# Optimization experiments

Hardware: AMD Instinct MI355X
Metric: run time of the kernel (lower is better)

The kernel has to match this reference:

```python
import jax, jax.numpy as jnp
import numpy as np

B, S, U, H, NT, MEM, FF = 2, 1024, 1024, 16, 32000, 576, 4096
D = U // H
VOCAB = 1024  # AdaptiveEmbedding(input_dim=units) in source -> vocab == units


def setup_inputs() -> dict:
    key = jax.random.key(0)
    ks = jax.random.split(key, 12)
    w = lambda k, shp, s=0.02: jax.random.normal(k, shp, jnp.float32) * s
    return dict(
        tokens=jax.random.randint(ks[0], (B, S), 0, VOCAB, dtype=jnp.int32),
        memory=jax.random.normal(ks[1], (B, MEM, U), jnp.float32),  # HelixMemory state (n_turns+memory_len)
        embed_table=w(ks[2], (VOCAB, U)),
        Wq=w(ks[3], (U, U)), Wkv=w(ks[4], (U, 2 * U)), Wr=w(ks[5], (U, U)), Wo=w(ks[6], (U, U)),
        bq=jnp.zeros((U,), jnp.float32), bkv=jnp.zeros((2 * U,), jnp.float32),
        br=jnp.zeros((U,), jnp.float32), bo=jnp.zeros((U,), jnp.float32),
        bias_context=w(ks[7], (U,)), bias_relative=w(ks[8], (U,)),
        ln1_g=jnp.ones((U,), jnp.float32), ln1_b=jnp.zeros((U,), jnp.float32),
        W1=w(ks[9], (U, FF)), b1=jnp.zeros((FF,), jnp.float32),
        W2=w(ks[10], (FF, U)), b2=jnp.zeros((U,), jnp.float32),
        ln2_g=jnp.ones((U,), jnp.float32), ln2_b=jnp.zeros((U,), jnp.float32),
        Wout=w(ks[11], (U, NT)), bout=jnp.zeros((NT,), jnp.float32),
    )


def _layer_norm(x, g, b, eps=1e-5):
    mu = jnp.mean(x, -1, keepdims=True)
    var = jnp.var(x, -1, keepdims=True)
    return (x - mu) * jax.lax.rsqrt(var + eps) * g + b


def _pos_embed(k_len, d):
    # Transformer-XL sinusoidal relative positions, descending k_len-1 .. 0
    pos = jnp.arange(k_len - 1, -1, -1, dtype=jnp.float32)
    inv_freq = 1.0 / (10000.0 ** (jnp.arange(0, d, 2, dtype=jnp.float32) / d))
    sinusoid = pos[:, None] * inv_freq[None, :]  # (k_len, d/2)
    return jnp.concatenate([jnp.sin(sinusoid), jnp.cos(sinusoid)], -1)  # (k_len, d)


def _rel_shift(x):
    # standard Transformer-XL relative shift: (B,H,S,K) -> shifted (B,H,S,K)
    b, h, s, k = x.shape
    x = jnp.pad(x, ((0, 0), (0, 0), (0, 0), (1, 0)))
    x = x.reshape(b, h, k + 1, s)[:, :, 1:, :]
    return x.reshape(b, h, s, k)


def _forward(tokens, memory, embed_table, Wq, Wkv, Wr, Wo, bq, bkv, br, bo,
             bias_context, bias_relative, ln1_g, ln1_b, W1, b1, W2, b2,
             ln2_g, ln2_b, Wout, bout):
    x = embed_table[tokens] * jnp.sqrt(jnp.float32(U))     # (B,S,U) embed + Scale
    full = jnp.concatenate([memory, x], axis=1)            # (B,K,U) memory-augmented keys/values
    k_len = full.shape[1]
    rel = _pos_embed(k_len, U)                             # (K,U) positional embedding

    q = x @ Wq + bq                                        # (B,S,U)
    kv = full @ Wkv + bkv                                  # (B,K,2U)
    r = (rel @ Wr + br).reshape(k_len, H, D)               # (K,H,D)
    k = kv[..., :U].reshape(B, k_len, H, D)
    v = kv[..., U:].reshape(B, k_len, H, D)
    q_c = (q + bias_context).reshape(B, S, H, D)           # q + u
    q_r = (q + bias_relative).reshape(B, S, H, D)          # q + v

    a_c = jnp.einsum('bihd,bjhd->bhij', q_c, k)            # content scores
    a_r = _rel_shift(jnp.einsum('bihd,jhd->bhij', q_r, r)) # position scores, rel-shifted
    att = (a_c + a_r) / jnp.sqrt(jnp.float32(D))
    # causal mask with memory offset: query i may attend keys j <= i + MEM
    mask = jnp.arange(k_len)[None, :] <= (jnp.arange(S)[:, None] + (k_len - S))
    att = jnp.where(mask[None, None], att, jnp.float32(-1e30))
    att = jax.nn.softmax(att, axis=-1)
    out = jnp.einsum('bhij,bjhd->bihd', att, v).reshape(B, S, U)
    out = out @ Wo + bo

    h1 = _layer_norm(x + out, ln1_g, ln1_b)                # Add + LayerNorm
    ff = jax.nn.relu(h1 @ W1 + b1) @ W2 + b2               # FeedForward
    h2 = _layer_norm(h1 + ff, ln2_g, ln2_b)
    return jax.nn.softmax(h2 @ Wout + bout, axis=-1)       # AdaptiveSoftmax head (div_val=1)


def reference(tokens, memory, embed_table, Wq, Wkv, Wr, Wo, bq, bkv, br, bo,
              bias_context, bias_relative, ln1_g, ln1_b, W1, b1, W2, b2,
              ln2_g, ln2_b, Wout, bout):
    return _forward(tokens, memory, embed_table, Wq, Wkv, Wr, Wo, bq, bkv, br, bo,
                    bias_context, bias_relative, ln1_g, ln1_b, W1, b1, W2, b2,
                    ln2_g, ln2_b, Wout, bout)
```

## Files before the change

kernel.cpp:

```cpp
#include <hip/hip_runtime.h>
#include <stdint.h>

typedef unsigned short u16;
typedef __bf16 bf16x8 __attribute__((ext_vector_type(8)));
typedef float f32x4 __attribute__((ext_vector_type(4)));

#define AS1 __attribute__((address_space(1)))
#define AS3 __attribute__((address_space(3)))

enum {
  B_ = 2, S_ = 1024, U_ = 1024, H_ = 16, D_ = 64,
  NT_ = 32000, MEM_ = 576, FF_ = 4096, KL_ = 1600,
  BS_ = 2048, BKL_ = 3200
};

__device__ __forceinline__ u16 f2b(float f) {
  uint32_t u = __builtin_bit_cast(uint32_t, f);
  u = (u + 0x7fffu + ((u >> 16) & 1u)) >> 16;
  return (u16)u;
}
__device__ __forceinline__ float b2f(u16 h) {
  uint32_t u = ((uint32_t)h) << 16;
  return __builtin_bit_cast(float, u);
}

__device__ __forceinline__ float block_sum(float v, volatile float* red) {
  int lane = threadIdx.x & 63, wv = threadIdx.x >> 6;
#pragma unroll
  for (int o = 32; o; o >>= 1) v += __shfl_xor(v, o, 64);
  if (lane == 0) red[wv] = v;
  __syncthreads();
  v = red[0] + red[1] + red[2] + red[3];
  __syncthreads();
  return v;
}
__device__ __forceinline__ float block_max(float v, volatile float* red) {
  int lane = threadIdx.x & 63, wv = threadIdx.x >> 6;
#pragma unroll
  for (int o = 32; o; o >>= 1) v = fmaxf(v, __shfl_xor(v, o, 64));
  if (lane == 0) red[wv] = v;
  __syncthreads();
  v = fmaxf(fmaxf(red[0], red[1]), fmaxf(red[2], red[3]));
  __syncthreads();
  return v;
}

__global__ __launch_bounds__(256)
void k_gemm(const u16* __restrict__ A, const u16* __restrict__ Bt,
            float* __restrict__ Cf, u16* __restrict__ Cb,
            const float* __restrict__ bias,
            int M, int N, int K, int lda, int ldb, int ldc,
            long long sAb, long long sAh, long long sBb, long long sBh,
            long long sCb, long long sCh, int nh, int mode)
{
  __shared__ __align__(16) u16 As[128][64];
  __shared__ __align__(16) u16 Bs[128][64];

  int z = blockIdx.z;
  int bb = z / nh, hh = z - bb * nh;
  A  += bb * sAb + hh * sAh;
  Bt += bb * sBb + hh * sBh;
  long long coff = bb * sCb + hh * sCh;

  int m0 = blockIdx.y * 128, n0 = blockIdx.x * 128;
  int t = threadIdx.x;
  int lane = t & 63, wave = t >> 6;
  int wm = (wave >> 1) * 64, wn = (wave & 1) * 64;
  int lrow = lane & 15, lq = lane >> 4;

  int srow = t >> 3;
  int scol = (t & 7) * 8;

  f32x4 acc[4][4];
#pragma unroll
  for (int i = 0; i < 4; i++)
#pragma unroll
    for (int j = 0; j < 4; j++) acc[i][j] = (f32x4){0.f, 0.f, 0.f, 0.f};

  for (int k0 = 0; k0 < K; k0 += 64) {
#pragma unroll
    for (int it = 0; it < 4; ++it) {
      int r = srow + 32 * it;
      int gr = m0 + r;
      if (gr < M)
        __builtin_amdgcn_global_load_lds(
            (const AS1 void*)(A + (long long)gr * lda + k0 + scol),
            (AS3 void*)(&As[r][scol]), 16, 0, 0);
      int gn = n0 + r;
      if (gn < N)
        __builtin_amdgcn_global_load_lds(
            (const AS1 void*)(Bt + (long long)gn * ldb + k0 + scol),
            (AS3 void*)(&Bs[r][scol]), 16, 0, 0);
    }
    __syncthreads();
#pragma unroll
    for (int ks = 0; ks < 2; ++ks) {
      int kk = ks * 32 + lq * 8;
      bf16x8 av[4], bv[4];
#pragma unroll
      for (int i = 0; i < 4; i++) av[i] = *(const bf16x8*)(&As[wm + i * 16 + lrow][kk]);
#pragma unroll
      for (int j = 0; j < 4; j++) bv[j] = *(const bf16x8*)(&Bs[wn + j * 16 + lrow][kk]);
#pragma unroll
      for (int i = 0; i < 4; i++)
#pragma unroll
        for (int j = 0; j < 4; j++)
          acc[i][j] = __builtin_amdgcn_mfma_f32_16x16x32_bf16(av[i], bv[j], acc[i][j], 0, 0, 0);
    }
    __syncthreads();
  }

#pragma unroll
  for (int j = 0; j < 4; j++) {
    int col = n0 + wn + j * 16 + lrow;
    if (col >= N) continue;
    float bvv = bias ? bias[col] : 0.f;
#pragma unroll
    for (int i = 0; i < 4; i++) {
      int row0 = m0 + wm + i * 16 + lq * 4;
#pragma unroll
      for (int r = 0; r < 4; r++) {
        int gr = row0 + r;
        if (gr >= M) continue;
        float v = acc[i][j][r] + bvv;
        if (mode == 2) {
          int tc = col - (S_ - 1 - gr);
          if (tc >= 0) {
            long long idx = coff + (long long)gr * ldc + tc;
            Cb[idx] = f2b(b2f(Cb[idx]) + v);
          }
          continue;
        }
        if (mode == 1) v = fmaxf(v, 0.f);
        long long idx = coff + (long long)gr * ldc + col;
        if (Cf) Cf[idx] = v;
        if (Cb) Cb[idx] = f2b(v);
      }
    }
  }
}

__global__ void k_embed(const int* __restrict__ tokens, const float* __restrict__ memory,
                        const float* __restrict__ table, u16* __restrict__ fullbf,
                        u16* __restrict__ xbf, float* __restrict__ xf)
{
  int row = blockIdx.x;
  int b = row / KL_, jk = row - b * KL_;
  int c = threadIdx.x * 4;
  u16* dst = fullbf + (size_t)row * U_ + c;
  if (jk < MEM_) {
    float4 v = *(const float4*)(memory + ((size_t)b * MEM_ + jk) * U_ + c);
    dst[0] = f2b(v.x); dst[1] = f2b(v.y); dst[2] = f2b(v.z); dst[3] = f2b(v.w);
  } else {
    int i = jk - MEM_;
    int tok = tokens[b * S_ + i];
    float4 v = *(const float4*)(table + (size_t)tok * U_ + c);
    v.x *= 32.f; v.y *= 32.f; v.z *= 32.f; v.w *= 32.f;
    dst[0] = f2b(v.x); dst[1] = f2b(v.y); dst[2] = f2b(v.z); dst[3] = f2b(v.w);
    size_t xi = ((size_t)b * S_ + i) * U_ + c;
    *(float4*)(xf + xi) = v;
    u16* xd = xbf + xi;
    xd[0] = f2b(v.x); xd[1] = f2b(v.y); xd[2] = f2b(v.z); xd[3] = f2b(v.w);
  }
}

__global__ void k_relpos(u16* __restrict__ relbf)
{
  int m = blockIdx.x;
  float pos = (float)(KL_ - 1 - m);
  const float c0 = 9.210340371976184f / 512.0f;
  for (int c = threadIdx.x; c < U_; c += 256) {
    int i = (c < 512) ? c : (c - 512);
    float inv = expf(-(float)i * c0);
    float arg = pos * inv;
    float v = (c < 512) ? sinf(arg) : cosf(arg);
    relbf[(size_t)m * U_ + c] = f2b(v);
  }
}

__global__ void k_qbias(const float* __restrict__ qf, const float* __restrict__ bc,
                        const float* __restrict__ br, u16* __restrict__ qc,
                        u16* __restrict__ qr)
{
  int c = threadIdx.x * 4;
  size_t idx = (size_t)blockIdx.x * U_ + c;
  float4 q = *(const float4*)(qf + idx);
  float4 vc = *(const float4*)(bc + c);
  float4 vr = *(const float4*)(br + c);
  qc[idx + 0] = f2b(q.x + vc.x); qc[idx + 1] = f2b(q.y + vc.y);
  qc[idx + 2] = f2b(q.z + vc.z); qc[idx + 3] = f2b(q.w + vc.w);
  qr[idx + 0] = f2b(q.x + vr.x); qr[idx + 1] = f2b(q.y + vr.y);
  qr[idx + 2] = f2b(q.z + vr.z); qr[idx + 3] = f2b(q.w + vr.w);
}

__global__ void k_transpose(const float* __restrict__ in, u16* __restrict__ out,
                            int R, int C)
{
  __shared__ float tile[32][33];
  int tx = threadIdx.x & 31, ty = threadIdx.x >> 5;
  int c0 = blockIdx.x * 32, r0 = blockIdx.y * 32;
#pragma unroll
  for (int i = 0; i < 4; i++) {
    int r = r0 + ty + i * 8;
    tile[ty + i * 8][tx] = in[(size_t)r * C + c0 + tx];
  }
  __syncthreads();
#pragma unroll
  for (int i = 0; i < 4; i++) {
    int c = c0 + ty + i * 8;
    out[(size_t)c * R + r0 + tx] = f2b(tile[tx][ty + i * 8]);
  }
}

__global__ void k_vt(const u16* __restrict__ kvbf, u16* __restrict__ vT)
{
  __shared__ u16 tile[32][33];
  int z = blockIdx.z;
  int b = z >> 4, h = z & 15;
  int tx = threadIdx.x & 31, ty = threadIdx.x >> 5;
  int j0 = blockIdx.x * 32, d0 = blockIdx.y * 32;
#pragma unroll
  for (int i = 0; i < 4; i++) {
    int j = j0 + ty + i * 8;
    tile[ty + i * 8][tx] = kvbf[((size_t)(b * KL_ + j)) * (2 * U_) + U_ + h * 64 + d0 + tx];
  }
  __syncthreads();
#pragma unroll
  for (int i = 0; i < 4; i++) {
    int d = d0 + ty + i * 8;
    vT[((size_t)(z * 64 + d)) * KL_ + j0 + tx] = tile[tx][ty + i * 8];
  }
}

__global__ void k_attnsm(u16* __restrict__ C1)
{
  __shared__ float red[4];
  int i = blockIdx.x, z = blockIdx.y;
  size_t base = ((size_t)z * S_ + i) * KL_;
  int jmax = i + MEM_;
  int t = threadIdx.x;
  float vloc[7];
  float lmax = -1e30f;
  int cnt = 0;
  for (int j = t; j < KL_; j += 256, ++cnt) {
    float v = -1e30f;
    if (j <= jmax) v = b2f(C1[base + j]) * 0.125f;
    vloc[cnt] = v;
    lmax = fmaxf(lmax, v);
  }
  float M = block_max(lmax, red);
  float lsum = 0.f;
  for (int c = 0; c < cnt; ++c) lsum += expf(vloc[c] - M);
  float L = block_sum(lsum, red);
  float inv = 1.f / L;
  cnt = 0;
  for (int j = t; j < KL_; j += 256, ++cnt)
    C1[base + j] = f2b(expf(vloc[cnt] - M) * inv);
}

__global__ void k_ln(const float* __restrict__ a, const float* __restrict__ b,
                     const float* __restrict__ g, const float* __restrict__ be,
                     float* __restrict__ yf, u16* __restrict__ yb)
{
  __shared__ float red[4];
  int c = threadIdx.x * 4;
  size_t idx = (size_t)blockIdx.x * U_ + c;
  float4 va = *(const float4*)(a + idx);
  float4 vb = *(const float4*)(b + idx);
  float s0 = va.x + vb.x, s1 = va.y + vb.y, s2 = va.z + vb.z, s3 = va.w + vb.w;
  float sum = block_sum(s0 + s1 + s2 + s3, red);
  float sq  = block_sum(s0 * s0 + s1 * s1 + s2 * s2 + s3 * s3, red);
  float mean = sum * (1.0f / U_);
  float var = sq * (1.0f / U_) - mean * mean;
  float rs = rsqrtf(var + 1e-5f);
  float4 vg = *(const float4*)(g + c);
  float4 vbe = *(const float4*)(be + c);
  float y0 = (s0 - mean) * rs * vg.x + vbe.x;
  float y1 = (s1 - mean) * rs * vg.y + vbe.y;
  float y2 = (s2 - mean) * rs * vg.z + vbe.z;
  float y3 = (s3 - mean) * rs * vg.w + vbe.w;
  if (yf) { float4 o = make_float4(y0, y1, y2, y3); *(float4*)(yf + idx) = o; }
  yb[idx + 0] = f2b(y0); yb[idx + 1] = f2b(y1);
  yb[idx + 2] = f2b(y2); yb[idx + 3] = f2b(y3);
}

__global__ void k_outsm(float* __restrict__ logits)
{
  __shared__ float redm[4], redl[4];
  int row = blockIdx.x, t = threadIdx.x;
  float* lp = logits + (size_t)row * NT_;
  float m = -1e30f, l = 0.f;
  for (int j = t; j < NT_; j += 256) {
    float x = lp[j];
    if (x > m) { l = l * expf(m - x) + 1.f; m = x; }
    else       { l += expf(x - m); }
  }
  int lane = t & 63, wv = t >> 6;
#pragma unroll
  for (int o = 32; o; o >>= 1) {
    float mo = __shfl_xor(m, o, 64), lo = __shfl_xor(l, o, 64);
    float mn = fmaxf(m, mo);
    l = l * expf(m - mn) + lo * expf(mo - mn);
    m = mn;
  }
  if (lane == 0) { redm[wv] = m; redl[wv] = l; }
  __syncthreads();
  float M = fmaxf(fmaxf(redm[0], redm[1]), fmaxf(redm[2], redm[3]));
  float L = redl[0] * expf(redm[0] - M) + redl[1] * expf(redm[1] - M) +
            redl[2] * expf(redm[2] - M) + redl[3] * expf(redm[3] - M);
  float inv = 1.f / L;
  for (int j = t; j < NT_; j += 256)
    lp[j] = expf(lp[j] - M) * inv;
}

static void gemm(hipStream_t st, const u16* A, const u16* Bt, float* Cf, u16* Cb,
                 const float* bias, int M, int N, int K, int lda, int ldb, int ldc,
                 long long sAb, long long sAh, long long sBb, long long sBh,
                 long long sCb, long long sCh, int nb, int nh, int mode)
{
  dim3 g((N + 127) / 128, (M + 127) / 128, nb * nh);
  k_gemm<<<g, 256, 0, st>>>(A, Bt, Cf, Cb, bias, M, N, K, lda, ldb, ldc,
                            sAb, sAh, sBb, sBh, sCb, sCh, nh, mode);
}

extern "C" void kernel_launch(void* const* d_in, const int* in_sizes, int n_in,
                              void* d_out, int out_size, void* d_ws, size_t ws_size,
                              hipStream_t stream)
{
  const int*   tokens = (const int*)d_in[0];
  const float* memory = (const float*)d_in[1];
  const float* table  = (const float*)d_in[2];
  const float* Wq   = (const float*)d_in[3];
  const float* Wkv  = (const float*)d_in[4];
  const float* Wr   = (const float*)d_in[5];
  const float* Wo   = (const float*)d_in[6];
  const float* bq   = (const float*)d_in[7];
  const float* bkv  = (const float*)d_in[8];
  const float* br   = (const float*)d_in[9];
  const float* bo   = (const float*)d_in[10];
  const float* bctx = (const float*)d_in[11];
  const float* brel = (const float*)d_in[12];
  const float* ln1g = (const float*)d_in[13];
  const float* ln1b = (const float*)d_in[14];
  const float* W1   = (const float*)d_in[15];
  const float* b1   = (const float*)d_in[16];
  const float* W2   = (const float*)d_in[17];
  const float* b2   = (const float*)d_in[18];
  const float* ln2g = (const float*)d_in[19];
  const float* ln2b = (const float*)d_in[20];
  const float* Wout = (const float*)d_in[21];
  const float* bout = (const float*)d_in[22];
  float* out = (float*)d_out;

  char* w = (char*)d_ws;
  size_t off = 0;
  auto carve = [&](size_t bytes) -> char* {
    char* p = w + off;
    off = (off + bytes + 255) & ~(size_t)255;
    return p;
  };

  u16*  WqT    = (u16*)carve((size_t)U_ * U_ * 2);
  u16*  WkvT   = (u16*)carve((size_t)2 * U_ * U_ * 2);
  u16*  WrT    = (u16*)carve((size_t)U_ * U_ * 2);
  u16*  WoT    = (u16*)carve((size_t)U_ * U_ * 2);
  u16*  W1T    = (u16*)carve((size_t)FF_ * U_ * 2);
  u16*  W2T    = (u16*)carve((size_t)U_ * FF_ * 2);
  float* xf    = (float*)carve((size_t)BS_ * U_ * 4);
  u16*  xbf    = (u16*)carve((size_t)BS_ * U_ * 2);
  u16*  fullbf = (u16*)carve((size_t)BKL_ * U_ * 2);
  u16*  relbf  = (u16*)carve((size_t)KL_ * U_ * 2);
  float* qf    = (float*)carve((size_t)BS_ * U_ * 4);
  u16*  qcbf   = (u16*)carve((size_t)BS_ * U_ * 2);
  u16*  qrbf   = (u16*)carve((size_t)BS_ * U_ * 2);
  u16*  kvbf   = (u16*)carve((size_t)BKL_ * 2 * U_ * 2);
  u16*  vT     = (u16*)carve((size_t)B_ * H_ * D_ * KL_ * 2);
  u16*  rW     = (u16*)carve((size_t)KL_ * U_ * 2);
  u16*  attout = (u16*)carve((size_t)BS_ * U_ * 2);
  float* of    = (float*)carve((size_t)BS_ * U_ * 4);
  float* h1f   = (float*)carve((size_t)BS_ * U_ * 4);
  u16*  h1bf   = (u16*)carve((size_t)BS_ * U_ * 2);
  u16*  ff1bf  = (u16*)carve((size_t)BS_ * FF_ * 2);
  float* ff2f  = (float*)carve((size_t)BS_ * U_ * 4);
  u16*  h2bf   = (u16*)carve((size_t)BS_ * U_ * 2);

  size_t scoreBytes = (size_t)B_ * H_ * S_ * KL_ * 2;
  char* big = carve(scoreBytes);
  u16* C1    = (u16*)big;
  u16* WoutT = (u16*)big;

  if (off > ws_size) return;

  k_transpose<<<dim3(U_ / 32, U_ / 32), 256, 0, stream>>>(Wq, WqT, U_, U_);
  k_transpose<<<dim3(2 * U_ / 32, U_ / 32), 256, 0, stream>>>(Wkv, WkvT, U_, 2 * U_);
  k_transpose<<<dim3(U_ / 32, U_ / 32), 256, 0, stream>>>(Wr, WrT, U_, U_);
  k_transpose<<<dim3(U_ / 32, U_ / 32), 256, 0, stream>>>(Wo, WoT, U_, U_);
  k_transpose<<<dim3(FF_ / 32, U_ / 32), 256, 0, stream>>>(W1, W1T, U_, FF_);
  k_transpose<<<dim3(U_ / 32, FF_ / 32), 256, 0, stream>>>(W2, W2T, FF_, U_);

  k_embed<<<dim3(BKL_), 256, 0, stream>>>(tokens, memory, table, fullbf, xbf, xf);
  k_relpos<<<dim3(KL_), 256, 0, stream>>>(relbf);

  gemm(stream, xbf, WqT, qf, nullptr, bq, BS_, U_, U_, U_, U_, U_,
       0, 0, 0, 0, 0, 0, 1, 1, 0);
  k_qbias<<<dim3(BS_), 256, 0, stream>>>(qf, bctx, brel, qcbf, qrbf);

  gemm(stream, fullbf, WkvT, nullptr, kvbf, bkv, BKL_, 2 * U_, U_, U_, U_, 2 * U_,
       0, 0, 0, 0, 0, 0, 1, 1, 0);
  k_vt<<<dim3(KL_ / 32, 2, B_ * H_), 256, 0, stream>>>(kvbf, vT);

  gemm(stream, relbf, WrT, nullptr, rW, br, KL_, U_, U_, U_, U_, U_,
       0, 0, 0, 0, 0, 0, 1, 1, 0);

  gemm(stream, qcbf, kvbf, nullptr, C1, nullptr,
       S_, KL_, D_, U_, 2 * U_, KL_,
       (long long)S_ * U_, 64, (long long)KL_ * 2 * U_, 64,
       (long long)H_ * S_ * KL_, (long long)S_ * KL_, B_, H_, 0);
  gemm(stream, qrbf, rW, nullptr, C1, nullptr,
       S_, KL_, D_, U_, U_, KL_,
       (long long)S_ * U_, 64, 0, 64,
       (long long)H_ * S_ * KL_, (long long)S_ * KL_, B_, H_, 2);

  k_attnsm<<<dim3(S_, B_ * H_), 256, 0, stream>>>(C1);

  gemm(stream, C1, vT, nullptr, attout, nullptr,
       S_, D_, KL_, KL_, KL_, U_,
       (long long)H_ * S_ * KL_, (long long)S_ * KL_,
       (long long)H_ * D_ * KL_, (long long)D_ * KL_,
       (long long)S_ * U_, 64, B_, H_, 0);

  gemm(stream, attout, WoT, of, nullptr, bo, BS_, U_, U_, U_, U_, U_,
       0, 0, 0, 0, 0, 0, 1, 1, 0);
  k_ln<<<dim3(BS_), 256, 0, stream>>>(xf, of, ln1g, ln1b, h1f, h1bf);

  gemm(stream, h1bf, W1T, nullptr, ff1bf, b1, BS_, FF_, U_, U_, U_, FF_,
       0, 0, 0, 0, 0, 0, 1, 1, 1);
  gemm(stream, ff1bf, W2T, ff2f, nullptr, b2, BS_, U_, FF_, FF_, FF_, U_,
       0, 0, 0, 0, 0, 0, 1, 1, 0);
  k_ln<<<dim3(BS_), 256, 0, stream>>>(h1f, ff2f, ln2g, ln2b, nullptr, h2bf);

  k_transpose<<<dim3(NT_ / 32, U_ / 32), 256, 0, stream>>>(Wout, WoutT, U_, NT_);

  gemm(stream, h2bf, WoutT, out, nullptr, bout, BS_, NT_, U_, U_, U_, NT_,
       0, 0, 0, 0, 0, 0, 1, 1, 0);
  k_outsm<<<dim3(BS_), 256, 0, stream>>>(out);
}
```

Before: 1.518 ms.

## Skip masked attention tiles and double-buffer LDS in the GEMM kernel

Adds causal tile skipping to the attention path. QK^T tiles lying entirely past the memory-offset causal boundary are skipped, and rel-shift score tiles that would never be written are skipped. The softmax processes only columns up to the block-row's causal limit, and the PV GEMM clamps its K extent to that limit. Separately, the GEMM kernel now double-buffers its LDS tiles so the next k-slice's global-to-LDS loads are issued before the MFMA work on the current slice. This doubles LDS use per block, which may lower occupancy, and relies on unwritten score regions never being read.

```diff
diff --git a/kernel.cpp b/kernel.cpp
--- a/kernel.cpp
+++ b/kernel.cpp
@@ -51,10 +51,16 @@
             const float* __restrict__ bias,
             int M, int N, int K, int lda, int ldb, int ldc,
             long long sAb, long long sAh, long long sBb, long long sBh,
-            long long sCb, long long sCh, int nh, int mode)
-{
-  __shared__ __align__(16) u16 As[128][64];
-  __shared__ __align__(16) u16 Bs[128][64];
+            long long sCb, long long sCh, int nh, int mode,
+            int kclamp_off, int flags)
+{
+  __shared__ __align__(16) u16 As[2][128][64];
+  __shared__ __align__(16) u16 Bs[2][128][64];
+
+  int m0 = blockIdx.y * 128, n0 = blockIdx.x * 128;
+
+  if ((flags & 1) && n0 > m0 + 127 + MEM_) return;
+  if (mode == 2 && n0 + m0 <= 768) return;
 
   int z = blockIdx.z;
   int bb = z / nh, hh = z - bb * nh;
@@ -62,7 +68,10 @@
   Bt += bb * sBb + hh * sBh;
   long long coff = bb * sCb + hh * sCh;
 
-  int m0 = blockIdx.y * 128, n0 = blockIdx.x * 128;
+  int Keff = K;
+  if (kclamp_off) { int kc = m0 + kclamp_off; if (kc < Keff) Keff = kc; }
+  int nk = Keff >> 6;
+
   int t = threadIdx.x;
   int lane = t & 63, wave = t >> 6;
   int wm = (wave >> 1) * 64, wn = (wave & 1) * 64;
@@ -71,13 +80,7 @@
   int srow = t >> 3;
   int scol = (t & 7) * 8;
 
-  f32x4 acc[4][4];
-#pragma unroll
-  for (int i = 0; i < 4; i++)
-#pragma unroll
-    for (int j = 0; j < 4; j++) acc[i][j] = (f32x4){0.f, 0.f, 0.f, 0.f};
-
-  for (int k0 = 0; k0 < K; k0 += 64) {
+  auto STAGE = [&](int buf, int k0) {
 #pragma unroll
     for (int it = 0; it < 4; ++it) {
       int r = srow + 32 * it;
@@ -85,22 +88,35 @@
       if (gr < M)
         __builtin_amdgcn_global_load_lds(
             (const AS1 void*)(A + (long long)gr * lda + k0 + scol),
-            (AS3 void*)(&As[r][scol]), 16, 0, 0);
+            (AS3 void*)(&As[buf][r][scol]), 16, 0, 0);
       int gn = n0 + r;
       if (gn < N)
         __builtin_amdgcn_global_load_lds(
             (const AS1 void*)(Bt + (long long)gn * ldb + k0 + scol),
-            (AS3 void*)(&Bs[r][scol]), 16, 0, 0);
+            (AS3 void*)(&Bs[buf][r][scol]), 16, 0, 0);
     }
-    __syncthreads();
+  };
+
+  f32x4 acc[4][4];
+#pragma unroll
+  for (int i = 0; i < 4; i++)
+#pragma unroll
+    for (int j = 0; j < 4; j++) acc[i][j] = (f32x4){0.f, 0.f, 0.f, 0.f};
+
+  STAGE(0, 0);
+  __syncthreads();
+
+  int cur = 0;
+  for (int kt = 0; kt < nk; ++kt) {
+    if (kt + 1 < nk) STAGE(cur ^ 1, (kt + 1) << 6);
 #pragma unroll
     for (int ks = 0; ks < 2; ++ks) {
       int kk = ks * 32 + lq * 8;
       bf16x8 av[4], bv[4];
 #pragma unroll
-      for (int i = 0; i < 4; i++) av[i] = *(const bf16x8*)(&As[wm + i * 16 + lrow][kk]);
-#pragma unroll
-      for (int j = 0; j < 4; j++) bv[j] = *(const bf16x8*)(&Bs[wn + j * 16 + lrow][kk]);
+      for (int i = 0; i < 4; i++) av[i] = *(const bf16x8*)(&As[cur][wm + i * 16 + lrow][kk]);
+#pragma unroll
+      for (int j = 0; j < 4; j++) bv[j] = *(const bf16x8*)(&Bs[cur][wn + j * 16 + lrow][kk]);
 #pragma unroll
       for (int i = 0; i < 4; i++)
 #pragma unroll
@@ -108,6 +124,7 @@
           acc[i][j] = __builtin_amdgcn_mfma_f32_16x16x32_bf16(av[i], bv[j], acc[i][j], 0, 0, 0);
     }
     __syncthreads();
+    cur ^= 1;
   }
 
 #pragma unroll
@@ -238,11 +255,13 @@
   int i = blockIdx.x, z = blockIdx.y;
   size_t base = ((size_t)z * S_ + i) * KL_;
   int jmax = i + MEM_;
+  int jhi = ((i >> 7) << 7) + MEM_ + 128;
+  if (jhi > KL_) jhi = KL_;
   int t = threadIdx.x;
   float vloc[7];
   float lmax = -1e30f;
   int cnt = 0;
-  for (int j = t; j < KL_; j += 256, ++cnt) {
+  for (int j = t; j < jhi; j += 256, ++cnt) {
     float v = -1e30f;
     if (j <= jmax) v = b2f(C1[base + j]) * 0.125f;
     vloc[cnt] = v;
@@ -254,7 +273,7 @@
   float L = block_sum(lsum, red);
   float inv = 1.f / L;
   cnt = 0;
-  for (int j = t; j < KL_; j += 256, ++cnt)
+  for (int j = t; j < jhi; j += 256, ++cnt)
     C1[base + j] = f2b(expf(vloc[cnt] - M) * inv);
 }
 
@@ -316,11 +335,13 @@
 static void gemm(hipStream_t st, const u16* A, const u16* Bt, float* Cf, u16* Cb,
                  const float* bias, int M, int N, int K, int lda, int ldb, int ldc,
                  long long sAb, long long sAh, long long sBb, long long sBh,
-                 long long sCb, long long sCh, int nb, int nh, int mode)
+                 long long sCb, long long sCh, int nb, int nh, int mode,
+                 int kclamp_off = 0, int flags = 0)
 {
   dim3 g((N + 127) / 128, (M + 127) / 128, nb * nh);
   k_gemm<<<g, 256, 0, st>>>(A, Bt, Cf, Cb, bias, M, N, K, lda, ldb, ldc,
-                            sAb, sAh, sBb, sBh, sCb, sCh, nh, mode);
+                            sAb, sAh, sBb, sBh, sCb, sCh, nh, mode,
+                            kclamp_off, flags);
 }
 
 extern "C" void kernel_launch(void* const* d_in, const int* in_sizes, int n_in,
@@ -415,7 +436,7 @@
   gemm(stream, qcbf, kvbf, nullptr, C1, nullptr,
        S_, KL_, D_, U_, 2 * U_, KL_,
        (long long)S_ * U_, 64, (long long)KL_ * 2 * U_, 64,
-       (long long)H_ * S_ * KL_, (long long)S_ * KL_, B_, H_, 0);
+       (long long)H_ * S_ * KL_, (long long)S_ * KL_, B_, H_, 0, 0, 1);
   gemm(stream, qrbf, rW, nullptr, C1, nullptr,
        S_, KL_, D_, U_, U_, KL_,
        (long long)S_ * U_, 64, 0, 64,
@@ -427,7 +448,7 @@
        S_, D_, KL_, KL_, KL_, U_,
        (long long)H_ * S_ * KL_, (long long)S_ * KL_,
        (long long)H_ * D_ * KL_, (long long)D_ * KL_,
-       (long long)S_ * U_, 64, B_, H_, 0);
+       (long long)S_ * U_, 64, B_, H_, 0, MEM_ + 128, 0);
 
   gemm(stream, attout, WoT, of, nullptr, bo, BS_, U_, U_, U_, U_, U_,
        0, 0, 0, 0, 0, 0, 1, 1, 0);
```

Measured after the change: 1.585 ms. 4.4% more time.

## Skip masked attention tiles and fuse output softmax statistics into GEMM epilogue

Applied to the files above, without the earlier changes.

The QK, positional-score, softmax and PV stages now skip tiles and K ranges that lie entirely beyond the causal-plus-memory mask. The positional GEMM also skips tiles whose rel-shifted outputs are unused. The vocab-projection GEMM gains a templated epilogue that writes per-tile row max and sum-exp partials. This lets the final softmax merge those partials instead of rescanning all logits for statistics, cutting one full read of the large output. The added risks are correctness of the skip bounds and reuse of the q buffers as scratch for the partials.

```diff
diff --git a/kernel.cpp b/kernel.cpp
--- a/kernel.cpp
+++ b/kernel.cpp
@@ -45,16 +45,24 @@
   return v;
 }
 
+template <int PART>
 __global__ __launch_bounds__(256)
 void k_gemm(const u16* __restrict__ A, const u16* __restrict__ Bt,
             float* __restrict__ Cf, u16* __restrict__ Cb,
             const float* __restrict__ bias,
             int M, int N, int K, int lda, int ldb, int ldc,
             long long sAb, long long sAh, long long sBb, long long sBh,
-            long long sCb, long long sCh, int nh, int mode)
+            long long sCb, long long sCh, int nh, int mode,
+            int kclamp_off, int flags,
+            float* __restrict__ Pm, float* __restrict__ Pl)
 {
   __shared__ __align__(16) u16 As[128][64];
   __shared__ __align__(16) u16 Bs[128][64];
+
+  int m0 = blockIdx.y * 128, n0 = blockIdx.x * 128;
+
+  if ((flags & 1) && n0 > m0 + 127 + MEM_) return;
+  if (mode == 2 && n0 + m0 <= 768) return;
 
   int z = blockIdx.z;
   int bb = z / nh, hh = z - bb * nh;
@@ -62,7 +70,9 @@
   Bt += bb * sBb + hh * sBh;
   long long coff = bb * sCb + hh * sCh;
 
-  int m0 = blockIdx.y * 128, n0 = blockIdx.x * 128;
+  int Keff = K;
+  if (kclamp_off) { int kc = m0 + kclamp_off; if (kc < Keff) Keff = kc; }
+
   int t = threadIdx.x;
   int lane = t & 63, wave = t >> 6;
   int wm = (wave >> 1) * 64, wn = (wave & 1) * 64;
@@ -77,7 +87,7 @@
 #pragma unroll
     for (int j = 0; j < 4; j++) acc[i][j] = (f32x4){0.f, 0.f, 0.f, 0.f};
 
-  for (int k0 = 0; k0 < K; k0 += 64) {
+  for (int k0 = 0; k0 < Keff; k0 += 64) {
 #pragma unroll
     for (int it = 0; it < 4; ++it) {
       int r = srow + 32 * it;
@@ -108,6 +118,47 @@
           acc[i][j] = __builtin_amdgcn_mfma_f32_16x16x32_bf16(av[i], bv[j], acc[i][j], 0, 0, 0);
     }
     __syncthreads();
+  }
+
+  if (PART) {
+    float* pmf = (float*)(&As[0][0]);
+    float* plf = pmf + 256;
+    int wh = wave & 1;
+#pragma unroll
+    for (int i = 0; i < 4; i++) {
+#pragma unroll
+      for (int r = 0; r < 4; r++) {
+        int row = wm + i * 16 + lq * 4 + r;
+        int gr = m0 + row;
+        float v[4];
+        float vmax = -1e30f;
+#pragma unroll
+        for (int j = 0; j < 4; j++) {
+          int col = n0 + wn + j * 16 + lrow;
+          v[j] = acc[i][j][r] + bias[col];
+          Cf[coff + (long long)gr * ldc + col] = v[j];
+          vmax = fmaxf(vmax, v[j]);
+        }
+#pragma unroll
+        for (int o = 1; o < 16; o <<= 1) vmax = fmaxf(vmax, __shfl_xor(vmax, o, 64));
+        float s = 0.f;
+#pragma unroll
+        for (int j = 0; j < 4; j++) s += expf(v[j] - vmax);
+#pragma unroll
+        for (int o = 1; o < 16; o <<= 1) s += __shfl_xor(s, o, 64);
+        if (lrow == 0) { pmf[row * 2 + wh] = vmax; plf[row * 2 + wh] = s; }
+      }
+    }
+    __syncthreads();
+    int nxt = gridDim.x;
+    for (int tt = t; tt < 128; tt += 256) {
+      float ma = pmf[tt * 2], mb = pmf[tt * 2 + 1];
+      float Mx = fmaxf(ma, mb);
+      float L = plf[tt * 2] * expf(ma - Mx) + plf[tt * 2 + 1] * expf(mb - Mx);
+      Pm[(size_t)(m0 + tt) * nxt + blockIdx.x] = Mx;
+      Pl[(size_t)(m0 + tt) * nxt + blockIdx.x] = L;
+    }
+    return;
   }
 
 #pragma unroll
@@ -238,11 +289,13 @@
   int i = blockIdx.x, z = blockIdx.y;
   size_t base = ((size_t)z * S_ + i) * KL_;
   int jmax = i + MEM_;
+  int jhi = ((i >> 7) << 7) + MEM_ + 128;
+  if (jhi > KL_) jhi = KL_;
   int t = threadIdx.x;
   float vloc[7];
   float lmax = -1e30f;
   int cnt = 0;
-  for (int j = t; j < KL_; j += 256, ++cnt) {
+  for (int j = t; j < jhi; j += 256, ++cnt) {
     float v = -1e30f;
     if (j <= jmax) v = b2f(C1[base + j]) * 0.125f;
     vloc[cnt] = v;
@@ -254,7 +307,7 @@
   float L = block_sum(lsum, red);
   float inv = 1.f / L;
   cnt = 0;
-  for (int j = t; j < KL_; j += 256, ++cnt)
+  for (int j = t; j < jhi; j += 256, ++cnt)
     C1[base + j] = f2b(expf(vloc[cnt] - M) * inv);
 }
 
@@ -284,16 +337,18 @@
   yb[idx + 2] = f2b(y2); yb[idx + 3] = f2b(y3);
 }
 
-__global__ void k_outsm(float* __restrict__ logits)
+__global__ void k_outsm2(float* __restrict__ logits,
+                         const float* __restrict__ Pm,
+                         const float* __restrict__ Pl, int nt)
 {
   __shared__ float redm[4], redl[4];
   int row = blockIdx.x, t = threadIdx.x;
-  float* lp = logits + (size_t)row * NT_;
   float m = -1e30f, l = 0.f;
-  for (int j = t; j < NT_; j += 256) {
-    float x = lp[j];
-    if (x > m) { l = l * expf(m - x) + 1.f; m = x; }
-    else       { l += expf(x - m); }
+  for (int j = t; j < nt; j += 256) {
+    float mj = Pm[(size_t)row * nt + j], lj = Pl[(size_t)row * nt + j];
+    float mn = fmaxf(m, mj);
+    l = l * expf(m - mn) + lj * expf(mj - mn);
+    m = mn;
   }
   int lane = t & 63, wv = t >> 6;
 #pragma unroll
@@ -309,6 +364,7 @@
   float L = redl[0] * expf(redm[0] - M) + redl[1] * expf(redm[1] - M) +
             redl[2] * expf(redm[2] - M) + redl[3] * expf(redm[3] - M);
   float inv = 1.f / L;
+  float* lp = logits + (size_t)row * NT_;
   for (int j = t; j < NT_; j += 256)
     lp[j] = expf(lp[j] - M) * inv;
 }
@@ -316,11 +372,19 @@
 static void gemm(hipStream_t st, const u16* A, const u16* Bt, float* Cf, u16* Cb,
                  const float* bias, int M, int N, int K, int lda, int ldb, int ldc,
                  long long sAb, long long sAh, long long sBb, long long sBh,
-                 long long sCb, long long sCh, int nb, int nh, int mode)
+                 long long sCb, long long sCh, int nb, int nh, int mode,
+                 int kclamp_off = 0, int flags = 0,
+                 float* Pm = nullptr, float* Pl = nullptr)
 {
   dim3 g((N + 127) / 128, (M + 127) / 128, nb * nh);
-  k_gemm<<<g, 256, 0, st>>>(A, Bt, Cf, Cb, bias, M, N, K, lda, ldb, ldc,
-                            sAb, sAh, sBb, sBh, sCb, sCh, nh, mode);
+  if (Pm)
+    k_gemm<1><<<g, 256, 0, st>>>(A, Bt, Cf, Cb, bias, M, N, K, lda, ldb, ldc,
+                                 sAb, sAh, sBb, sBh, sCb, sCh, nh, mode,
+                                 kclamp_off, flags, Pm, Pl);
+  else
+    k_gemm<0><<<g, 256, 0, st>>>(A, Bt, Cf, Cb, bias, M, N, K, lda, ldb, ldc,
+                                 sAb, sAh, sBb, sBh, sCb, sCh, nh, mode,
+                                 kclamp_off, flags, nullptr, nullptr);
 }
 
 extern "C" void kernel_launch(void* const* d_in, const int* in_sizes, int n_in,
@@ -389,6 +453,9 @@
   u16* C1    = (u16*)big;
   u16* WoutT = (u16*)big;
 
+  float* Pm = (float*)qcbf;
+  float* Pl = (float*)qrbf;
+
   if (off > ws_size) return;
 
   k_transpose<<<dim3(U_ / 32, U_ / 32), 256, 0, stream>>>(Wq, WqT, U_, U_);
@@ -415,7 +482,7 @@
   gemm(stream, qcbf, kvbf, nullptr, C1, nullptr,
        S_, KL_, D_, U_, 2 * U_, KL_,
        (long long)S_ * U_, 64, (long long)KL_ * 2 * U_, 64,
-       (long long)H_ * S_ * KL_, (long long)S_ * KL_, B_, H_, 0);
+       (long long)H_ * S_ * KL_, (long long)S_ * KL_, B_, H_, 0, 0, 1);
   gemm(stream, qrbf, rW, nullptr, C1, nullptr,
        S_, KL_, D_, U_, U_, KL_,
        (long long)S_ * U_, 64, 0, 64,
@@ -427,7 +494,7 @@
        S_, D_, KL_, KL_, KL_, U_,
        (long long)H_ * S_ * KL_, (long long)S_ * KL_,
        (long long)H_ * D_ * KL_, (long long)D_ * KL_,
-       (long long)S_ * U_, 64, B_, H_, 0);
+       (long long)S_ * U_, 64, B_, H_, 0, MEM_ + 128, 0);
 
   gemm(stream, attout, WoT, of, nullptr, bo, BS_, U_, U_, U_, U_, U_,
        0, 0, 0, 0, 0, 0, 1, 1, 0);
@@ -442,6 +509,6 @@
   k_transpose<<<dim3(NT_ / 32, U_ / 32), 256, 0, stream>>>(Wout, WoutT, U_, NT_);
 
   gemm(stream, h2bf, WoutT, out, nullptr, bout, BS_, NT_, U_, U_, U_, NT_,
-       0, 0, 0, 0, 0, 0, 1, 1, 0);
-  k_outsm<<<dim3(BS_), 256, 0, stream>>>(out);
-}
+       0, 0, 0, 0, 0, 0, 1, 1, 0, 0, 0, Pm, Pl);
+  k_outsm2<<<dim3(BS_), 256, 0, stream>>>(out, Pm, Pl, NT_ / 128);
+}
```

New measurement: 1.380 ms. 9.1% less time.
